# Kernel optimization log

Hardware: AMD Instinct MI355X
Metric: run time of the kernel (lower is better)

## Reference

```python
import jax, jax.numpy as jnp
import numpy as np

NODE_DIM = 256
OUTPUT_DIM = 256
NUM_HOPS = 4
NUM_NODES = 25000
NUM_EDGES = 400000
NUM_TYPES = 10
FEAT_DIM = 32


def setup_inputs() -> dict:
    key = jax.random.key(0)
    ks = jax.random.split(key, 12)
    nodes = jax.random.normal(ks[0], (NUM_NODES, FEAT_DIM), dtype=jnp.float32)
    edges = jax.random.randint(ks[1], (2, NUM_EDGES), 0, NUM_NODES, dtype=jnp.int64)
    node_types = jax.random.randint(ks[2], (NUM_NODES,), 0, NUM_TYPES, dtype=jnp.int64)
    s = 0.02
    type_emb = jax.random.normal(ks[3], (NUM_TYPES, NODE_DIM), dtype=jnp.float32) * s
    W_proj = jax.random.normal(ks[4], (FEAT_DIM, NODE_DIM), dtype=jnp.float32) * s
    b_proj = jnp.zeros((NODE_DIM,), dtype=jnp.float32)
    W_msg = jax.random.normal(ks[5], (NUM_HOPS, 2 * NODE_DIM, NODE_DIM), dtype=jnp.float32) * s
    b_msg = jnp.zeros((NUM_HOPS, NODE_DIM), dtype=jnp.float32)
    W_upd = jax.random.normal(ks[6], (NUM_HOPS, 2 * NODE_DIM, NODE_DIM), dtype=jnp.float32) * s
    b_upd = jnp.zeros((NUM_HOPS, NODE_DIM), dtype=jnp.float32)
    W_out = jax.random.normal(ks[7], (NODE_DIM, OUTPUT_DIM), dtype=jnp.float32) * s
    b_out = jnp.zeros((OUTPUT_DIM,), dtype=jnp.float32)
    return {"nodes": nodes, "edges": edges, "node_types": node_types,
            "type_emb": type_emb, "W_proj": W_proj, "b_proj": b_proj,
            "W_msg": W_msg, "b_msg": b_msg, "W_upd": W_upd, "b_upd": b_upd,
            "W_out": W_out, "b_out": b_out}


def reference(nodes, edges, node_types, type_emb, W_proj, b_proj,
              W_msg, b_msg, W_upd, b_upd, W_out, b_out):
    n = nodes.shape[0]
    src, dst = edges[0], edges[1]
    # initial node states: linear proj + type embedding
    h = nodes @ W_proj + b_proj + type_emb[node_types]  # [N, D]
    for i in range(NUM_HOPS):
        edge_feat = jnp.concatenate([h[src], h[dst]], axis=1)      # [E, 2D]
        messages = edge_feat @ W_msg[i] + b_msg[i]                 # [E, D]
        agg = jax.ops.segment_sum(messages, dst, num_segments=n)   # [N, D]
        h = jax.nn.relu(jnp.concatenate([h, agg], axis=1) @ W_upd[i] + b_upd[i])
    graph_embedding = jnp.max(h, axis=0)                           # [D]
    return graph_embedding @ W_out + b_out                          # [output_dim]
```

## Files before the change

kernel.cpp:

```cpp
#include <hip/hip_runtime.h>
#include <hip/hip_bf16.h>

#define NDIM 256
#define FDIM 32
#define HOPS 4
#define NPB 8

typedef __attribute__((ext_vector_type(8))) short short8;
typedef __attribute__((ext_vector_type(4))) float f32x4;
typedef __attribute__((ext_vector_type(2))) float f32x2;

__device__ inline float b2f(unsigned short u) {
    union { unsigned int i; float f; } v; v.i = ((unsigned int)u) << 16; return v.f;
}
__device__ inline unsigned short f2b(float f) {
    union { float f; unsigned int i; } v; v.f = f;
    unsigned int r = v.i + 0x7FFF + ((v.i >> 16) & 1);
    return (unsigned short)(r >> 16);
}
__device__ inline unsigned char f2fp8(float v) {
    return (unsigned char)(__builtin_amdgcn_cvt_pk_fp8_f32(v, v, 0, false) & 0xFF);
}

__global__ __launch_bounds__(256) void prep_mega_kernel(
        const int* __restrict__ dst, int* __restrict__ deg, int E, int histB,
        const float* __restrict__ Wm, const float* __restrict__ Wu,
        const float* __restrict__ bm,
        unsigned short* __restrict__ WtB,
        unsigned short* __restrict__ Am, unsigned short* __restrict__ BmT,
        float* __restrict__ cvec, int* __restrict__ geInt,
        unsigned char* __restrict__ h8row,
        const float* __restrict__ nodes, const int* __restrict__ node_types,
        const float* __restrict__ type_emb, const float* __restrict__ W_proj,
        const float* __restrict__ b_proj,
        unsigned short* __restrict__ h, unsigned char* __restrict__ h8, int n) {
    __shared__ float T[32][33];
    __shared__ float sb[256];
    int b = blockIdx.x;
    int t = threadIdx.x;

    if (b < histB) {
        int e = b * 256 + t;
        if (e < E) atomicAdd(&deg[dst[e]], 1);
    } else if (b < histB + 773) {
        int bb = b - histB;
        if (bb < 256) {
            int hop = bb >> 6;
            int rem = bb & 63;
            int k0 = (rem & 7) * 32, n0 = (rem >> 3) * 32;
            const float* src = Wu + (size_t)hop * 512 * 256;
            unsigned short* dstp = WtB + (size_t)hop * 256 * 256;
            int tr = t >> 5, tc = t & 31;
#pragma unroll
            for (int r = 0; r < 4; ++r) {
                int k = tr + r * 8;
                T[tc][k] = src[(size_t)(k0 + k) * 256 + n0 + tc];
            }
            __syncthreads();
#pragma unroll
            for (int r = 0; r < 4; ++r) {
                int nn = tr + r * 8;
                dstp[(size_t)(n0 + nn) * 256 + k0 + tc] = f2b(T[nn][tc]);
            }
        } else if (bb < 260) {
            int hop = bb - 256;
            sb[t] = bm[hop * 256 + t];
            __syncthreads();
            const float* B = Wu + (size_t)hop * 512 * 256 + (size_t)256 * 256;
            float acc = 0.f;
#pragma unroll 8
            for (int j = 0; j < 256; ++j) acc += sb[j] * B[(size_t)j * 256 + t];
            cvec[hop * 256 + t] = acc;
        } else if (bb == 260) {
            geInt[t] = 0;
            h8row[t] = 0;
        } else if (bb < 517) {
            size_t base = (size_t)(bb - 261) * 2048 + (size_t)t * 8;
            float4 a0 = *(const float4*)(Wm + base);
            float4 a1 = *(const float4*)(Wm + base + 4);
            ushort4 o0, o1;
            o0.x = f2b(a0.x); o0.y = f2b(a0.y); o0.z = f2b(a0.z); o0.w = f2b(a0.w);
            o1.x = f2b(a1.x); o1.y = f2b(a1.y); o1.z = f2b(a1.z); o1.w = f2b(a1.w);
            *(ushort4*)(Am + base) = o0;
            *(ushort4*)(Am + base + 4) = o1;
        } else {
            int tb = bb - 517;
            int hop = tb >> 6;
            int rem = tb & 63;
            int j0 = (rem & 7) * 32, n0 = (rem >> 3) * 32;
            const float* srcp = Wu + (size_t)hop * 512 * 256 + (size_t)256 * 256;
            unsigned short* dstp = BmT + (size_t)hop * 256 * 256;
            int tr = t >> 5, tc = t & 31;
#pragma unroll
            for (int r = 0; r < 4; ++r) {
                int j = tr + r * 8;
                T[tc][j] = srcp[(size_t)(j0 + j) * 256 + n0 + tc];
            }
            __syncthreads();
#pragma unroll
            for (int r = 0; r < 4; ++r) {
                int nn = tr + r * 8;
                dstp[(size_t)(n0 + nn) * 256 + j0 + tc] = f2b(T[nn][tc]);
            }
        }
    } else {
        int v0 = (b - histB - 773) * NPB;
        {
            int j = t >> 5, f = t & 31;
            int v = v0 + j;
            sb[t] = (v < n) ? nodes[(size_t)v * FDIM + f] : 0.f;
        }
        __syncthreads();
        float acc[NPB];
#pragma unroll
        for (int j = 0; j < NPB; ++j) {
            int v = v0 + j;
            acc[j] = (v < n) ? (b_proj[t] + type_emb[(size_t)node_types[v] * NDIM + t]) : 0.f;
        }
#pragma unroll 4
        for (int k = 0; k < FDIM; ++k) {
            float wv = W_proj[(size_t)k * NDIM + t];
#pragma unroll
            for (int j = 0; j < NPB; ++j)
                acc[j] += sb[j * FDIM + k] * wv;
        }
#pragma unroll
        for (int j = 0; j < NPB; ++j) {
            int v = v0 + j;
            if (v < n) {
                h[(size_t)v * NDIM + t] = f2b(acc[j]);
                h8[(size_t)v * NDIM + t] = f2fp8(acc[j]);
            }
        }
    }
}

__global__ __launch_bounds__(1024) void scan1_mm_kernel(
        const int* __restrict__ deg, int* __restrict__ rowptr,
        int* __restrict__ bsum, int nch, int n,
        const unsigned short* __restrict__ Am, const unsigned short* __restrict__ BmT,
        unsigned short* __restrict__ WtA, unsigned short* __restrict__ WtC) {
    int t = threadIdx.x;
    int b = blockIdx.x;
    if (b < nch) {
        __shared__ int wsum[16];
        int i = b * 1024 + t;
        int v = 0;
        if (i < n) v = (deg[i] + 7) & ~7;
        int lane = t & 63, wid = t >> 6;
        int x = v;
#pragma unroll
        for (int d = 1; d < 64; d <<= 1) {
            int u = __shfl_up(x, d, 64);
            if (lane >= d) x += u;
        }
        if (lane == 63) wsum[wid] = x;
        __syncthreads();
        if (wid == 0) {
            int ws = (lane < 16) ? wsum[lane] : 0;
#pragma unroll
            for (int d = 1; d < 16; d <<= 1) {
                int u = __shfl_up(ws, d, 64);
                if (lane >= d) ws += u;
            }
            if (lane < 16) wsum[lane] = ws;
        }
        __syncthreads();
        int excl = (wid > 0 ? wsum[wid - 1] : 0) + x - v;
        if (i < n) rowptr[i] = excl;
        if (t == 1023) bsum[b] = wsum[15];
        return;
    }

    int m = b - nch;
    int hop = m >> 1, which = m & 1;
    const unsigned short* A = Am + (size_t)m * 65536;
    const unsigned short* B = BmT + (size_t)hop * 65536;
    unsigned short* W = (which ? WtC : WtA) + (size_t)hop * 65536;
    int wave = t >> 6, lane = t & 63;
    int l16 = lane & 15, quad = lane >> 4;
    int k0 = (wave & 3) * 64;
    int n0 = (wave >> 2) * 64;
    f32x4 acc[4][4];
#pragma unroll
    for (int i = 0; i < 4; ++i)
#pragma unroll
        for (int j = 0; j < 4; ++j) acc[i][j] = (f32x4)(0.f);

    for (int j0 = 0; j0 < 256; j0 += 32) {
        short8 af[4], bfr[4];
#pragma unroll
        for (int kt = 0; kt < 4; ++kt)
            af[kt] = *(const short8*)(A + (size_t)(k0 + kt * 16 + l16) * 256 + j0 + quad * 8);
#pragma unroll
        for (int nt = 0; nt < 4; ++nt)
            bfr[nt] = *(const short8*)(B + (size_t)(n0 + nt * 16 + l16) * 256 + j0 + quad * 8);
#pragma unroll
        for (int kt = 0; kt < 4; ++kt)
#pragma unroll
            for (int nt = 0; nt < 4; ++nt)
                acc[kt][nt] = __builtin_amdgcn_mfma_f32_16x16x32_bf16(af[kt], bfr[nt], acc[kt][nt], 0, 0, 0);
    }
#pragma unroll
    for (int kt = 0; kt < 4; ++kt)
#pragma unroll
        for (int nt = 0; nt < 4; ++nt) {
            int k = k0 + kt * 16 + quad * 4;
            int nn = n0 + nt * 16 + l16;
            ushort4 o;
            o.x = f2b(acc[kt][nt][0]); o.y = f2b(acc[kt][nt][1]);
            o.z = f2b(acc[kt][nt][2]); o.w = f2b(acc[kt][nt][3]);
            *(ushort4*)&W[(size_t)nn * 256 + k] = o;
        }
}

__global__ __launch_bounds__(1024) void scan2_kernel(
        int* __restrict__ rowptr, int* __restrict__ cursor,
        const int* __restrict__ bsum, int nch, int n) {
    __shared__ int soff, stot;
    int t = threadIdx.x;
    int b = blockIdx.x;
    if (t < 64) {
        int s = (t < nch) ? bsum[t] : 0;
        int x = s;
#pragma unroll
        for (int d = 1; d < 64; d <<= 1) {
            int u = __shfl_up(x, d, 64);
            if (t >= d) x += u;
        }
        if (t == 63) stot = x;
        if (t == b) soff = x - s;
    }
    __syncthreads();
    int i = b * 1024 + t;
    if (i < n) {
        int r = rowptr[i] + soff;
        rowptr[i] = r;
        cursor[i] = r;
    }
    if (b == 0 && t == 0) rowptr[n] = stot;
}

__global__ void fillpad_kernel(const int* __restrict__ src, const int* __restrict__ dst,
                               int* __restrict__ cursor,
                               const int* __restrict__ rowptr, const int* __restrict__ deg,
                               int* __restrict__ col, int E, int fillB, int n) {
    int b = blockIdx.x;
    int t = threadIdx.x;
    if (b < fillB) {
        int e = b * 256 + t;
        if (e < E) {
            int d = dst[e];
            int p = atomicAdd(&cursor[d], 1);
            col[p] = src[e];
        }
    } else {
        int v = (b - fillB) * 256 + t;
        if (v < n) {
            int s = rowptr[v] + deg[v];
            int e0 = rowptr[v + 1];
            for (int i = s; i < e0; ++i) col[i] = n;
        }
    }
}

__global__ __launch_bounds__(256) void agg_kernel(const unsigned char* __restrict__ h8,
                                                  const int* __restrict__ rowptr,
                                                  const int* __restrict__ col,
                                                  unsigned short* __restrict__ S, int n) {
    int wave = threadIdx.x >> 6;
    int lane = threadIdx.x & 63;
    int half = lane >> 5;
    int hl = lane & 31;
    int v = blockIdx.x * 8 + wave * 2 + half;
    if (v >= n) return;
    int beg = rowptr[v], end = rowptr[v + 1];
    float a[8];
#pragma unroll
    for (int e = 0; e < 8; ++e) a[e] = 0.f;
    int cofs = hl * 8;
    for (int i = beg; i < end; i += 8) {
        int cc[8];
#pragma unroll
        for (int j = 0; j < 8; ++j) cc[j] = col[i + j];
        uint2 x[8];
#pragma unroll
        for (int j = 0; j < 8; ++j)
            x[j] = *(const uint2*)(h8 + (size_t)cc[j] * NDIM + cofs);
#pragma unroll
        for (int j = 0; j < 8; ++j) {
            f32x2 p0 = __builtin_amdgcn_cvt_pk_f32_fp8(x[j].x, false);
            f32x2 p1 = __builtin_amdgcn_cvt_pk_f32_fp8(x[j].x, true);
            f32x2 p2 = __builtin_amdgcn_cvt_pk_f32_fp8(x[j].y, false);
            f32x2 p3 = __builtin_amdgcn_cvt_pk_f32_fp8(x[j].y, true);
            a[0] += p0[0]; a[1] += p0[1]; a[2] += p1[0]; a[3] += p1[1];
            a[4] += p2[0]; a[5] += p2[1]; a[6] += p3[0]; a[7] += p3[1];
        }
    }
    uint4 o;
    unsigned short* op = (unsigned short*)&o;
#pragma unroll
    for (int e = 0; e < 8; ++e) op[e] = f2b(a[e]);
    *(uint4*)&S[(size_t)v * NDIM + cofs] = o;
}

#define BM 128
#define BN 64
#define BK 64
#define ASTR (BK + 8)

template <bool LAST>
__global__ __launch_bounds__(256) void gemm_hop_kernel(const unsigned short* __restrict__ S,
                                                       const unsigned short* __restrict__ hcur,
                                                       const int* __restrict__ deg,
                                                       const unsigned short* __restrict__ WtA,
                                                       const unsigned short* __restrict__ WtB,
                                                       const unsigned short* __restrict__ WtC,
                                                       const float* __restrict__ bupd,
                                                       const float* __restrict__ cvec,
                                                       unsigned short* __restrict__ Out,
                                                       unsigned char* __restrict__ Out8,
                                                       int* __restrict__ geInt, int n) {
    __shared__ unsigned short As[BM][ASTR];
    __shared__ unsigned short Bs[BN][ASTR];
    __shared__ unsigned short Cs[BN][ASTR];
    __shared__ int smax[BN];
    int t = threadIdx.x;
    int lane = t & 63;
    int w = t >> 6;
    int wm = w >> 1, wn = w & 1;
    int quad = lane >> 4, l16 = lane & 15;
    int row0 = blockIdx.x * BM;
    int n0 = blockIdx.y * BN;

    if (LAST) {
        if (t < BN) smax[t] = 0;
    }

    f32x4 acc1[4][2], acc2[4][2];
#pragma unroll
    for (int i = 0; i < 4; ++i)
#pragma unroll
        for (int j = 0; j < 2; ++j) { acc1[i][j] = (f32x4)(0.f); acc2[i][j] = (f32x4)(0.f); }

    for (int k0 = 0; k0 < NDIM; k0 += BK) {
        __syncthreads();
#pragma unroll
        for (int h2 = 0; h2 < 4; ++h2) {
            int c = t + h2 * 256;
            int r = c >> 3;
            int ko = (c & 7) * 8;
            int grow = row0 + r; if (grow >= n) grow = n - 1;
            *(uint4*)&As[r][ko] = *(const uint4*)(S + (size_t)grow * NDIM + k0 + ko);
        }
#pragma unroll
        for (int h2 = 0; h2 < 2; ++h2) {
            int c = t + h2 * 256;
            int r = c >> 3;
            int ko = (c & 7) * 8;
            *(uint4*)&Bs[r][ko] = *(const uint4*)(WtA + (size_t)(n0 + r) * NDIM + k0 + ko);
        }
        __syncthreads();
#pragma unroll
        for (int ks = 0; ks < BK; ks += 32) {
            short8 af[4], bf[2];
#pragma unroll
            for (int mt = 0; mt < 4; ++mt)
                af[mt] = *(const short8*)&As[wm * 64 + mt * 16 + l16][ks + quad * 8];
#pragma unroll
            for (int nt = 0; nt < 2; ++nt)
                bf[nt] = *(const short8*)&Bs[wn * 32 + nt * 16 + l16][ks + quad * 8];
#pragma unroll
            for (int mt = 0; mt < 4; ++mt)
#pragma unroll
                for (int nt = 0; nt < 2; ++nt)
                    acc1[mt][nt] = __builtin_amdgcn_mfma_f32_16x16x32_bf16(af[mt], bf[nt], acc1[mt][nt], 0, 0, 0);
        }
    }
    for (int k0 = 0; k0 < NDIM; k0 += BK) {
        __syncthreads();
#pragma unroll
        for (int h2 = 0; h2 < 4; ++h2) {
            int c = t + h2 * 256;
            int r = c >> 3;
            int ko = (c & 7) * 8;
            int grow = row0 + r; if (grow >= n) grow = n - 1;
            *(uint4*)&As[r][ko] = *(const uint4*)(hcur + (size_t)grow * NDIM + k0 + ko);
        }
#pragma unroll
        for (int h2 = 0; h2 < 2; ++h2) {
            int c = t + h2 * 256;
            int r = c >> 3;
            int ko = (c & 7) * 8;
            size_t widx = (size_t)(n0 + r) * NDIM + k0 + ko;
            *(uint4*)&Bs[r][ko] = *(const uint4*)(WtB + widx);
            *(uint4*)&Cs[r][ko] = *(const uint4*)(WtC + widx);
        }
        __syncthreads();
#pragma unroll
        for (int ks = 0; ks < BK; ks += 32) {
            short8 af[4], bf[2], cf[2];
#pragma unroll
            for (int mt = 0; mt < 4; ++mt)
                af[mt] = *(const short8*)&As[wm * 64 + mt * 16 + l16][ks + quad * 8];
#pragma unroll
            for (int nt = 0; nt < 2; ++nt) {
                bf[nt] = *(const short8*)&Bs[wn * 32 + nt * 16 + l16][ks + quad * 8];
                cf[nt] = *(const short8*)&Cs[wn * 32 + nt * 16 + l16][ks + quad * 8];
            }
#pragma unroll
            for (int mt = 0; mt < 4; ++mt)
#pragma unroll
                for (int nt = 0; nt < 2; ++nt) {
                    acc1[mt][nt] = __builtin_amdgcn_mfma_f32_16x16x32_bf16(af[mt], bf[nt], acc1[mt][nt], 0, 0, 0);
                    acc2[mt][nt] = __builtin_amdgcn_mfma_f32_16x16x32_bf16(af[mt], cf[nt], acc2[mt][nt], 0, 0, 0);
                }
        }
    }
#pragma unroll
    for (int mt = 0; mt < 4; ++mt) {
#pragma unroll
        for (int nt = 0; nt < 2; ++nt) {
            int lcol = wn * 32 + nt * 16 + l16;
            int col = n0 + lcol;
            float bu = bupd[col];
            float cv = cvec[col];
            float cmax = 0.f;
#pragma unroll
            for (int r = 0; r < 4; ++r) {
                int row = row0 + wm * 64 + mt * 16 + quad * 4 + r;
                if (row < n) {
                    float dg = (float)deg[row];
                    float v = fmaxf(acc1[mt][nt][r] + dg * (acc2[mt][nt][r] + cv) + bu, 0.f);
                    Out[(size_t)row * NDIM + col] = f2b(v);
                    if (!LAST) Out8[(size_t)row * NDIM + col] = f2fp8(v);
                    if (LAST) cmax = fmaxf(cmax, v);
                }
            }
            if (LAST) atomicMax(&smax[lcol], __float_as_int(cmax));
        }
    }
    if (LAST) {
        __syncthreads();
        if (t < BN) atomicMax(&geInt[n0 + t], smax[t]);
    }
}

__global__ __launch_bounds__(1024) void out_kernel(const float* __restrict__ ge,
                                                   const float* __restrict__ W_out,
                                                   const float* __restrict__ b_out,
                                                   float* __restrict__ out) {
    __shared__ float red[4][NDIM];
    int t = threadIdx.x & 255;
    int g = threadIdx.x >> 8;
    float acc = 0.f;
#pragma unroll 8
    for (int kk = 0; kk < 64; ++kk) {
        int k = g * 64 + kk;
        acc += ge[k] * W_out[k * NDIM + t];
    }
    red[g][t] = acc;
    __syncthreads();
    if (g == 0)
        out[t] = b_out[t] + red[0][t] + red[1][t] + red[2][t] + red[3][t];
}

extern "C" void kernel_launch(void* const* d_in, const int* in_sizes, int n_in,
                              void* d_out, int out_size, void* d_ws, size_t ws_size,
                              hipStream_t stream) {
    const float* nodes      = (const float*)d_in[0];
    const int*   edges      = (const int*)d_in[1];
    const int*   node_types = (const int*)d_in[2];
    const float* type_emb   = (const float*)d_in[3];
    const float* W_proj     = (const float*)d_in[4];
    const float* b_proj     = (const float*)d_in[5];
    const float* W_msg      = (const float*)d_in[6];
    const float* b_msg      = (const float*)d_in[7];
    const float* W_upd      = (const float*)d_in[8];
    const float* b_upd      = (const float*)d_in[9];
    const float* W_out      = (const float*)d_in[10];
    const float* b_out      = (const float*)d_in[11];

    int n = in_sizes[2];
    int E = in_sizes[1] / 2;
    const int* src = edges;
    const int* dst = edges + E;

    size_t off = 0;
    auto alloc = [&](size_t bytes) {
        void* p = (char*)d_ws + off;
        off += (bytes + 255) & ~(size_t)255;
        return p;
    };
    int* deg    = (int*)alloc((size_t)(n + 4096) * 4);
    int* rowptr = (int*)alloc((size_t)(n + 1) * 4);
    int* cursor = (int*)alloc((size_t)n * 4);
    int* bsum   = (int*)alloc((size_t)256 * 4);
    int* col    = (int*)alloc((size_t)(E + 8 * n) * 4);
    unsigned short* WtA = (unsigned short*)alloc((size_t)HOPS * 256 * 256 * 2);
    unsigned short* WtB = (unsigned short*)alloc((size_t)HOPS * 256 * 256 * 2);
    unsigned short* WtC = (unsigned short*)alloc((size_t)HOPS * 256 * 256 * 2);
    unsigned short* Am  = (unsigned short*)alloc((size_t)8 * 256 * 256 * 2);
    unsigned short* BmT = (unsigned short*)alloc((size_t)HOPS * 256 * 256 * 2);
    float* cvec = (float*)alloc((size_t)HOPS * 256 * 4);
    int* geInt  = (int*)alloc((size_t)256 * 4);
    unsigned short* hA  = (unsigned short*)alloc((size_t)(n + 1) * NDIM * 2);
    unsigned short* hB  = (unsigned short*)alloc((size_t)(n + 1) * NDIM * 2);
    unsigned short* Sb  = (unsigned short*)alloc((size_t)n * NDIM * 2);
    unsigned char* h8   = (unsigned char*)alloc((size_t)(n + 1) * NDIM);

    hipMemsetAsync(deg, 0, (size_t)(n + 4096) * 4, stream);
    int eb = (E + 255) / 256;
    int pb = (n + 255) / 256;
    int ib = (n + NPB - 1) / NPB;
    int nch = (n + 1023) / 1024;
    prep_mega_kernel<<<eb + 773 + ib, 256, 0, stream>>>(
        dst, deg, E, eb,
        W_msg, W_upd, b_msg, WtB, Am, BmT, cvec, geInt, h8 + (size_t)n * NDIM,
        nodes, node_types, type_emb, W_proj, b_proj, hA, h8, n);
    scan1_mm_kernel<<<nch + 8, 1024, 0, stream>>>(deg, rowptr, bsum, nch, n, Am, BmT, WtA, WtC);
    scan2_kernel<<<nch, 1024, 0, stream>>>(rowptr, cursor, bsum, nch, n);
    fillpad_kernel<<<eb + pb, 256, 0, stream>>>(src, dst, cursor, rowptr, deg, col, E, eb, n);

    unsigned short* h  = hA;
    unsigned short* ho = hB;
    int gx = (n + BM - 1) / BM;
    dim3 ggrid(gx, NDIM / BN);
    for (int i = 0; i < HOPS; ++i) {
        agg_kernel<<<(n + 7) / 8, 256, 0, stream>>>(h8, rowptr, col, Sb, n);
        size_t wofs = (size_t)i * 256 * 256;
        if (i == HOPS - 1)
            gemm_hop_kernel<true><<<ggrid, 256, 0, stream>>>(
                Sb, h, deg, WtA + wofs, WtB + wofs, WtC + wofs,
                b_upd + (size_t)i * NDIM, cvec + (size_t)i * NDIM, ho, h8, geInt, n);
        else
            gemm_hop_kernel<false><<<ggrid, 256, 0, stream>>>(
                Sb, h, deg, WtA + wofs, WtB + wofs, WtC + wofs,
                b_upd + (size_t)i * NDIM, cvec + (size_t)i * NDIM, ho, h8, geInt, n);
        unsigned short* tmp = h; h = ho; ho = tmp;
    }
    out_kernel<<<1, 1024, 0, stream>>>((const float*)geInt, W_out, b_out, (float*)d_out);
}
```

Measured before the change: 377.6 us.

## Load GEMM tiles directly into LDS with XOR-swizzled layout

Replaces the register-staged global-to-shared copies in the hop GEMM with direct global_load_lds transfers. The padded shared-memory rows become an unpadded layout whose 16-byte chunks are XOR-swizzled by row to avoid bank conflicts. The aim is fewer VGPRs and instructions on the load path and less LDS footprint. Correctness depends on each wave's LDS destination mapping matching the swizzle, and on the barrier covering completion of the asynchronous LDS writes.

```diff
diff --git a/kernel.cpp b/kernel.cpp
--- a/kernel.cpp
+++ b/kernel.cpp
@@ -307,7 +307,6 @@
 #define BM 128
 #define BN 64
 #define BK 64
-#define ASTR (BK + 8)
 
 template <bool LAST>
 __global__ __launch_bounds__(256) void gemm_hop_kernel(const unsigned short* __restrict__ S,
@@ -321,9 +320,9 @@
                                                        unsigned short* __restrict__ Out,
                                                        unsigned char* __restrict__ Out8,
                                                        int* __restrict__ geInt, int n) {
-    __shared__ unsigned short As[BM][ASTR];
-    __shared__ unsigned short Bs[BN][ASTR];
-    __shared__ unsigned short Cs[BN][ASTR];
+    __shared__ unsigned short As[BM * BK];
+    __shared__ unsigned short Bs[BN * BK];
+    __shared__ unsigned short Cs[BN * BK];
     __shared__ int smax[BN];
     int t = threadIdx.x;
     int lane = t & 63;
@@ -349,27 +348,37 @@
         for (int h2 = 0; h2 < 4; ++h2) {
             int c = t + h2 * 256;
             int r = c >> 3;
-            int ko = (c & 7) * 8;
+            int cb = (c & 7) ^ (r & 7);
             int grow = row0 + r; if (grow >= n) grow = n - 1;
-            *(uint4*)&As[r][ko] = *(const uint4*)(S + (size_t)grow * NDIM + k0 + ko);
+            __builtin_amdgcn_global_load_lds(
+                (const unsigned int*)(S + (size_t)grow * NDIM + k0 + cb * 8),
+                (unsigned int*)(As + (size_t)(h2 * 256 + w * 64) * 8), 16, 0, 0);
         }
 #pragma unroll
         for (int h2 = 0; h2 < 2; ++h2) {
             int c = t + h2 * 256;
             int r = c >> 3;
-            int ko = (c & 7) * 8;
-            *(uint4*)&Bs[r][ko] = *(const uint4*)(WtA + (size_t)(n0 + r) * NDIM + k0 + ko);
+            int cb = (c & 7) ^ (r & 7);
+            __builtin_amdgcn_global_load_lds(
+                (const unsigned int*)(WtA + (size_t)(n0 + r) * NDIM + k0 + cb * 8),
+                (unsigned int*)(Bs + (size_t)(h2 * 256 + w * 64) * 8), 16, 0, 0);
         }
         __syncthreads();
 #pragma unroll
         for (int ks = 0; ks < BK; ks += 32) {
             short8 af[4], bf[2];
 #pragma unroll
-            for (int mt = 0; mt < 4; ++mt)
-                af[mt] = *(const short8*)&As[wm * 64 + mt * 16 + l16][ks + quad * 8];
-#pragma unroll
-            for (int nt = 0; nt < 2; ++nt)
-                bf[nt] = *(const short8*)&Bs[wn * 32 + nt * 16 + l16][ks + quad * 8];
+            for (int mt = 0; mt < 4; ++mt) {
+                int ar = wm * 64 + mt * 16 + l16;
+                int acb = ((ks >> 3) + quad) ^ (ar & 7);
+                af[mt] = *(const short8*)&As[ar * BK + acb * 8];
+            }
+#pragma unroll
+            for (int nt = 0; nt < 2; ++nt) {
+                int br = wn * 32 + nt * 16 + l16;
+                int bcb = ((ks >> 3) + quad) ^ (br & 7);
+                bf[nt] = *(const short8*)&Bs[br * BK + bcb * 8];
+            }
 #pragma unroll
             for (int mt = 0; mt < 4; ++mt)
 #pragma unroll
@@ -383,30 +392,41 @@
         for (int h2 = 0; h2 < 4; ++h2) {
             int c = t + h2 * 256;
             int r = c >> 3;
-            int ko = (c & 7) * 8;
+            int cb = (c & 7) ^ (r & 7);
             int grow = row0 + r; if (grow >= n) grow = n - 1;
-            *(uint4*)&As[r][ko] = *(const uint4*)(hcur + (size_t)grow * NDIM + k0 + ko);
+            __builtin_amdgcn_global_load_lds(
+                (const unsigned int*)(hcur + (size_t)grow * NDIM + k0 + cb * 8),
+                (unsigned int*)(As + (size_t)(h2 * 256 + w * 64) * 8), 16, 0, 0);
         }
 #pragma unroll
         for (int h2 = 0; h2 < 2; ++h2) {
             int c = t + h2 * 256;
             int r = c >> 3;
-            int ko = (c & 7) * 8;
-            size_t widx = (size_t)(n0 + r) * NDIM + k0 + ko;
-            *(uint4*)&Bs[r][ko] = *(const uint4*)(WtB + widx);
-            *(uint4*)&Cs[r][ko] = *(const uint4*)(WtC + widx);
+            int cb = (c & 7) ^ (r & 7);
+            size_t widx = (size_t)(n0 + r) * NDIM + k0 + cb * 8;
+            __builtin_amdgcn_global_load_lds(
+                (const unsigned int*)(WtB + widx),
+                (unsigned int*)(Bs + (size_t)(h2 * 256 + w * 64) * 8), 16, 0, 0);
+            __builtin_amdgcn_global_load_lds(
+                (const unsigned int*)(WtC + widx),
+                (unsigned int*)(Cs + (size_t)(h2 * 256 + w * 64) * 8), 16, 0, 0);
         }
         __syncthreads();
 #pragma unroll
         for (int ks = 0; ks < BK; ks += 32) {
             short8 af[4], bf[2], cf[2];
 #pragma unroll
-            for (int mt = 0; mt < 4; ++mt)
-                af[mt] = *(const short8*)&As[wm * 64 + mt * 16 + l16][ks + quad * 8];
+            for (int mt = 0; mt < 4; ++mt) {
+                int ar = wm * 64 + mt * 16 + l16;
+                int acb = ((ks >> 3) + quad) ^ (ar & 7);
+                af[mt] = *(const short8*)&As[ar * BK + acb * 8];
+            }
 #pragma unroll
             for (int nt = 0; nt < 2; ++nt) {
-                bf[nt] = *(const short8*)&Bs[wn * 32 + nt * 16 + l16][ks + quad * 8];
-                cf[nt] = *(const short8*)&Cs[wn * 32 + nt * 16 + l16][ks + quad * 8];
+                int br = wn * 32 + nt * 16 + l16;
+                int bcb = ((ks >> 3) + quad) ^ (br & 7);
+                bf[nt] = *(const short8*)&Bs[br * BK + bcb * 8];
+                cf[nt] = *(const short8*)&Cs[br * BK + bcb * 8];
             }
 #pragma unroll
             for (int mt = 0; mt < 4; ++mt)
```

Measured after the change: 365.6 us. 1.03x faster.
